# Kernel optimization log

Measured on AMD Instinct MI355X. Metric: run time of the kernel, lower is better.

The kernel has to match this reference:

```python
import jax, jax.numpy as jnp
import numpy as np

N, M, D = 16384, 1024, 1024


def setup_inputs() -> dict:
    key = jax.random.key(0)
    kq, kp = jax.random.split(key)
    query = jax.random.normal(kq, (N, D), dtype=jnp.float32)
    proto = jax.random.normal(kp, (M, D), dtype=jnp.float32)
    return {"query": query, "proto": proto}


def reference(query, proto):
    # Pairwise squared euclidean: ||q||^2 - 2 q.p + ||p||^2  (same math as
    # the expand+pow+sum in compute_euclidean, but without the [N,M,D] blowup).
    q2 = jnp.sum(query * query, axis=-1, keepdims=True)          # [N,1]
    p2 = jnp.sum(proto * proto, axis=-1)                          # [M]
    qp = jnp.einsum('nd,md->nm', query, proto)                    # [N,M]
    dists = q2 - 2.0 * qp + p2[None, :]                           # [N,M]
    # Original applies F.softmax(-dists, dim=1) (named log_p_y but is softmax).
    return jax.nn.softmax(-dists, axis=1)
```

## Files before the change

kernel.cpp:

```cpp
#include <hip/hip_runtime.h>
#include <stdint.h>

#define N_Q 16384
#define M_P 1024
#define D_K 1024

typedef __attribute__((ext_vector_type(8))) __bf16 bf16x8;
typedef __attribute__((ext_vector_type(4))) float floatx4;
typedef __attribute__((ext_vector_type(4))) unsigned int uint4v;

#define AS1 __attribute__((address_space(1)))
#define AS3 __attribute__((address_space(3)))

__device__ __forceinline__ unsigned short f2bf(float f) {
    unsigned int u = __float_as_uint(f);
    u += 0x7fffu + ((u >> 16) & 1u);
    return (unsigned short)(u >> 16);
}
__device__ __forceinline__ float bf2f(unsigned short h) {
    return __uint_as_float(((unsigned int)h) << 16);
}

__device__ __forceinline__ void split_chunk(floatx4 f0, floatx4 f1,
                                            uint4v* hi, uint4v* lo) {
    float e[8] = {f0.x, f0.y, f0.z, f0.w, f1.x, f1.y, f1.z, f1.w};
    unsigned int hb[4], lb[4];
#pragma unroll
    for (int p = 0; p < 4; ++p) {
        unsigned int u0 = __float_as_uint(e[2 * p]);
        unsigned int u1 = __float_as_uint(e[2 * p + 1]);
        hb[p] = __builtin_amdgcn_perm(u1, u0, 0x07060302);
        float l0 = e[2 * p]     - __uint_as_float(u0 & 0xffff0000u);
        float l1 = e[2 * p + 1] - __uint_as_float(u1 & 0xffff0000u);
        lb[p] = __builtin_amdgcn_perm(__float_as_uint(l1), __float_as_uint(l0),
                                      0x07060302);
    }
    uint4v h = {hb[0], hb[1], hb[2], hb[3]};
    uint4v l = {lb[0], lb[1], lb[2], lb[3]};
    *hi = h;
    *lo = l;
}

__global__ __launch_bounds__(256) void convert_proto_kernel(
    const float* __restrict__ proto, unsigned short* __restrict__ ph,
    unsigned short* __restrict__ pl, float* __restrict__ p2) {
    __shared__ float sred[4];
    int m = blockIdx.x;
    int t = threadIdx.x;
    size_t base4 = (size_t)m * (D_K / 4) + t;
    float4 v = ((const float4*)proto)[base4];
    ushort4 h, l;
    h.x = f2bf(v.x); l.x = f2bf(v.x - bf2f(h.x));
    h.y = f2bf(v.y); l.y = f2bf(v.y - bf2f(h.y));
    h.z = f2bf(v.z); l.z = f2bf(v.z - bf2f(h.z));
    h.w = f2bf(v.w); l.w = f2bf(v.w - bf2f(h.w));
    ((ushort4*)ph)[base4] = h;
    ((ushort4*)pl)[base4] = l;
    float sq = v.x * v.x + v.y * v.y + v.z * v.z + v.w * v.w;
#pragma unroll
    for (int off = 1; off < 64; off <<= 1) sq += __shfl_xor(sq, off);
    if ((t & 63) == 0) sred[t >> 6] = sq;
    __syncthreads();
    if (t == 0) p2[m] = sred[0] + sred[1] + sred[2] + sred[3];
}

__global__ __launch_bounds__(512, 2) void gemm_logits_kernel(
    const float* __restrict__ query,
    const unsigned short* __restrict__ ph, const unsigned short* __restrict__ pl,
    const float* __restrict__ p2, float* __restrict__ out) {
    __shared__ unsigned short sAh[2][16 * 512];
    __shared__ unsigned short sAl[2][16 * 512];
    __shared__ unsigned short sBh[2][16 * 512];
    __shared__ unsigned short sBl[2][16 * 512];

    const int tid = threadIdx.x;
    const int wave = tid >> 6;
    const int lane = tid & 63;
    const int wr = wave >> 2;
    const int wc = wave & 3;

    const int b = blockIdx.x;
    const int v = (b & 7) * 32 + (b >> 3);
    const int colt = v >> 6;
    const int rowt = v & 63;
    const int row0 = rowt * 256;
    const int col0 = colt * 256;

    const int rlB = lane >> 2;
    const int cioB = (lane & 3) ^ ((lane >> 3) & 3);
    const int halfB = wave >> 2;
    const int sgB = wave & 3;
    const unsigned short* gB = (halfB ? pl : ph)
        + (size_t)(col0 + sgB * 64 + rlB) * D_K + cioB * 8;

    const int rlA = lane >> 2;
    const int cA = lane & 3;
    const AS1 float* gA = (const AS1 float*)query
        + (size_t)(row0 + wave * 32 + rlA) * D_K + cA * 8;
    const int wroff = (4 * rlA + (cA ^ ((rlA >> 1) & 3))) * 8;

    const int rsel = lane & 15;
    const int kq = lane >> 4;
    const int fragoff = (4 * rsel + (kq ^ ((rsel >> 1) & 3))) * 8;

    floatx4 zero = {0.0f, 0.0f, 0.0f, 0.0f};
    floatx4 acc[8][4];
#pragma unroll
    for (int i = 0; i < 8; ++i)
#pragma unroll
        for (int j = 0; j < 4; ++j) acc[i][j] = zero;

    floatx4 f0[2], f1[2];
    bf16x8 bh[4], bl[4];
    bf16x8 ah[2][2], al[2][2];

    auto issueA = [&](int kb) {
#pragma unroll
        for (int s = 0; s < 2; ++s) {
            const AS1 float* p = gA + (size_t)(s * 16) * D_K + kb;
            f0[s] = *(const AS1 floatx4*)p;
            f1[s] = *(const AS1 floatx4*)(p + 4);
        }
    };
    auto issueB = [&](int kb, int nxt) {
        unsigned short* dstB = (halfB ? sBl[nxt] : sBh[nxt]) + sgB * 4 * 512;
#pragma unroll
        for (int s = 0; s < 4; ++s)
            __builtin_amdgcn_global_load_lds(
                (const AS1 unsigned int*)(const void*)(gB + (size_t)(s * 16) * D_K + kb),
                (AS3 unsigned int*)(void*)(dstB + s * 512), 16, 0, 0);
    };
    auto writeA = [&](int nxt, int s) {
        uint4v hi, lo;
        split_chunk(f0[s], f1[s], &hi, &lo);
        const int off = (wave * 2 + s) * 512 + wroff;
        *(uint4v*)(sAh[nxt] + off) = hi;
        *(uint4v*)(sAl[nxt] + off) = lo;
    };
    auto ldBfrag = [&](int cur) {
#pragma unroll
        for (int j = 0; j < 4; ++j) {
            const int boff = (wc * 4 + j) * 512 + fragoff;
            bh[j] = *(const bf16x8*)(sBh[cur] + boff);
            bl[j] = *(const bf16x8*)(sBl[cur] + boff);
        }
    };
    auto ldA = [&](int cur, int i0, int set) {
#pragma unroll
        for (int t = 0; t < 2; ++t) {
            const int aoff = (wr * 8 + i0 + t) * 512 + fragoff;
            ah[set][t] = *(const bf16x8*)(sAh[cur] + aoff);
            al[set][t] = *(const bf16x8*)(sAl[cur] + aoff);
        }
    };
    auto mfma2 = [&](int i0, int set) {
#pragma unroll
        for (int j = 0; j < 4; ++j)
#pragma unroll
            for (int t = 0; t < 2; ++t) {
                acc[i0 + t][j] = __builtin_amdgcn_mfma_f32_16x16x32_bf16(ah[set][t], bh[j], acc[i0 + t][j], 0, 0, 0);
                acc[i0 + t][j] = __builtin_amdgcn_mfma_f32_16x16x32_bf16(ah[set][t], bl[j], acc[i0 + t][j], 0, 0, 0);
                acc[i0 + t][j] = __builtin_amdgcn_mfma_f32_16x16x32_bf16(al[set][t], bh[j], acc[i0 + t][j], 0, 0, 0);
            }
    };

#define LGKM_MFMA(n, i0, set)                                   \
    asm volatile("s_waitcnt lgkmcnt(" #n ")" ::: "memory");     \
    __builtin_amdgcn_sched_barrier(0);                          \
    __builtin_amdgcn_s_setprio(1);                              \
    mfma2(i0, set);                                             \
    __builtin_amdgcn_s_setprio(0);

    auto stepf = [&](int kbnB, int kbnA, int cur, int nxt, bool pfB, bool pfA) {
        if (pfB) issueB(kbnB, nxt);
        ldBfrag(cur);
        ldA(cur, 0, 0);
        ldA(cur, 2, 1);
        LGKM_MFMA(4, 0, 0)
        ldA(cur, 4, 0);
        LGKM_MFMA(4, 2, 1)
        ldA(cur, 6, 1);
        LGKM_MFMA(4, 4, 0)
        if (pfB) { writeA(nxt, 0); writeA(nxt, 1); }
        if (pfA) issueA(kbnA);
        asm volatile("s_waitcnt lgkmcnt(0)" ::: "memory");
        if (pfB) {
            if (pfA) asm volatile("s_waitcnt vmcnt(4)" ::: "memory");
            else     asm volatile("s_waitcnt vmcnt(0)" ::: "memory");
        }
        __builtin_amdgcn_sched_barrier(0);
        __builtin_amdgcn_s_setprio(1);
        mfma2(6, 1);
        __builtin_amdgcn_s_setprio(0);
        __builtin_amdgcn_s_barrier();
    };

    issueA(0);
    issueB(0, 0);
    writeA(0, 0);
    writeA(0, 1);
    issueA(32);
    asm volatile("s_waitcnt lgkmcnt(0)" ::: "memory");
    asm volatile("s_waitcnt vmcnt(4)" ::: "memory");
    __builtin_amdgcn_s_barrier();

    for (int kt = 0; kt < 30; kt += 2) {
        stepf((kt + 1) * 32, (kt + 2) * 32, 0, 1, true, true);
        stepf((kt + 2) * 32, (kt + 3) * 32, 1, 0, true, true);
    }
    stepf(31 * 32, 0, 0, 1, true, false);
    stepf(0, 0, 1, 0, false, false);

#undef LGKM_MFMA

#pragma unroll
    for (int j = 0; j < 4; ++j) {
        const int gc = col0 + wc * 64 + j * 16 + rsel;
        const float p2v = p2[gc];
#pragma unroll
        for (int i = 0; i < 8; ++i) {
            const int gr = row0 + wr * 128 + i * 16 + kq * 4;
#pragma unroll
            for (int r = 0; r < 4; ++r) {
                out[(size_t)(gr + r) * M_P + gc] = 2.0f * acc[i][j][r] - p2v;
            }
        }
    }
}

__global__ __launch_bounds__(256) void naive_logits_kernel(
    const float* __restrict__ query, const float* __restrict__ proto,
    float* __restrict__ out) {
    __shared__ float qs[D_K];
    int n = blockIdx.x;
    int t = threadIdx.x;
    ((float4*)qs)[t] = ((const float4*)(query + (size_t)n * D_K))[t];
    __syncthreads();
    float acc[4] = {0.f, 0.f, 0.f, 0.f};
    float pp[4] = {0.f, 0.f, 0.f, 0.f};
    for (int d = 0; d < D_K; d += 4) {
        float4 qv = *(const float4*)(qs + d);
#pragma unroll
        for (int j = 0; j < 4; ++j) {
            const float4 pv = *(const float4*)(proto + (size_t)(t + 256 * j) * D_K + d);
            acc[j] += qv.x * pv.x + qv.y * pv.y + qv.z * pv.z + qv.w * pv.w;
            pp[j] += pv.x * pv.x + pv.y * pv.y + pv.z * pv.z + pv.w * pv.w;
        }
    }
#pragma unroll
    for (int j = 0; j < 4; ++j)
        out[(size_t)n * M_P + t + 256 * j] = 2.0f * acc[j] - pp[j];
}

__global__ __launch_bounds__(256) void softmax_kernel(float* __restrict__ out) {
    const int lane = threadIdx.x & 63;
    int n = blockIdx.x * 4 + (threadIdx.x >> 6);
    for (int it = 0; it < 2; ++it, n += 8192) {
        float* row = out + (size_t)n * M_P;
        floatx4 v[4];
#pragma unroll
        for (int k = 0; k < 4; ++k)
            v[k] = *((const floatx4*)row + k * 64 + lane);
        float mx = fmaxf(fmaxf(v[0].x, v[0].y), fmaxf(v[0].z, v[0].w));
#pragma unroll
        for (int k = 1; k < 4; ++k)
            mx = fmaxf(mx, fmaxf(fmaxf(v[k].x, v[k].y), fmaxf(v[k].z, v[k].w)));
#pragma unroll
        for (int off = 1; off < 64; off <<= 1) mx = fmaxf(mx, __shfl_xor(mx, off));
        float s = 0.0f;
#pragma unroll
        for (int k = 0; k < 4; ++k) {
            v[k].x = __expf(v[k].x - mx);
            v[k].y = __expf(v[k].y - mx);
            v[k].z = __expf(v[k].z - mx);
            v[k].w = __expf(v[k].w - mx);
            s += v[k].x + v[k].y + v[k].z + v[k].w;
        }
#pragma unroll
        for (int off = 1; off < 64; off <<= 1) s += __shfl_xor(s, off);
        const float inv = 1.0f / s;
#pragma unroll
        for (int k = 0; k < 4; ++k) {
            floatx4 o;
            o.x = v[k].x * inv; o.y = v[k].y * inv;
            o.z = v[k].z * inv; o.w = v[k].w * inv;
            __builtin_nontemporal_store(o, (floatx4*)row + k * 64 + lane);
        }
    }
}

extern "C" void kernel_launch(void* const* d_in, const int* in_sizes, int n_in,
                              void* d_out, int out_size, void* d_ws, size_t ws_size,
                              hipStream_t stream) {
    const float* query = (const float*)d_in[0];
    const float* proto = (const float*)d_in[1];
    float* out = (float*)d_out;

    const size_t pElems = (size_t)M_P * D_K;
    const size_t needed = pElems * 2 * 2 + M_P * 4;

    if (ws_size >= needed) {
        unsigned short* ph = (unsigned short*)d_ws;
        unsigned short* pl = ph + pElems;
        float* p2 = (float*)(pl + pElems);

        convert_proto_kernel<<<M_P, 256, 0, stream>>>(proto, ph, pl, p2);
        gemm_logits_kernel<<<(N_Q / 256) * (M_P / 256), 512, 0, stream>>>(
            query, ph, pl, p2, out);
    } else {
        naive_logits_kernel<<<N_Q, 256, 0, stream>>>(query, proto, out);
    }
    softmax_kernel<<<2048, 256, 0, stream>>>(out);
}
```

Before: 198.1 us.

## Triple-buffer B tiles in LDS to prefetch two k-steps ahead

```diff
diff --git a/kernel.cpp b/kernel.cpp
--- a/kernel.cpp
+++ b/kernel.cpp
@@ -70,8 +70,8 @@
     const float* __restrict__ p2, float* __restrict__ out) {
     __shared__ unsigned short sAh[2][16 * 512];
     __shared__ unsigned short sAl[2][16 * 512];
-    __shared__ unsigned short sBh[2][16 * 512];
-    __shared__ unsigned short sBl[2][16 * 512];
+    __shared__ unsigned short sBh[3][16 * 512];
+    __shared__ unsigned short sBl[3][16 * 512];
 
     const int tid = threadIdx.x;
     const int wave = tid >> 6;
@@ -122,8 +122,8 @@
             f1[s] = *(const AS1 floatx4*)(p + 4);
         }
     };
-    auto issueB = [&](int kb, int nxt) {
-        unsigned short* dstB = (halfB ? sBl[nxt] : sBh[nxt]) + sgB * 4 * 512;
+    auto issueB = [&](int kb, int dst) {
+        unsigned short* dstB = (halfB ? sBl[dst] : sBh[dst]) + sgB * 4 * 512;
 #pragma unroll
         for (int s = 0; s < 4; ++s)
             __builtin_amdgcn_global_load_lds(
@@ -137,12 +137,12 @@
         *(uint4v*)(sAh[nxt] + off) = hi;
         *(uint4v*)(sAl[nxt] + off) = lo;
     };
-    auto ldBfrag = [&](int cur) {
+    auto ldBfrag = [&](int curB) {
 #pragma unroll
         for (int j = 0; j < 4; ++j) {
             const int boff = (wc * 4 + j) * 512 + fragoff;
-            bh[j] = *(const bf16x8*)(sBh[cur] + boff);
-            bl[j] = *(const bf16x8*)(sBl[cur] + boff);
+            bh[j] = *(const bf16x8*)(sBh[curB] + boff);
+            bl[j] = *(const bf16x8*)(sBl[curB] + boff);
         }
     };
     auto ldA = [&](int cur, int i0, int set) {
@@ -171,45 +171,52 @@
     mfma2(i0, set);                                             \
     __builtin_amdgcn_s_setprio(0);
 
-    auto stepf = [&](int kbnB, int kbnA, int cur, int nxt, bool pfB, bool pfA) {
-        if (pfB) issueB(kbnB, nxt);
-        ldBfrag(cur);
-        ldA(cur, 0, 0);
-        ldA(cur, 2, 1);
+    auto stepf = [&](int kb2, int curA, int nxtA, int curB, int dstB,
+                     bool pfB2, bool pfA2, bool pfW) {
+        if (pfB2) issueB(kb2, dstB);
+        ldBfrag(curB);
+        ldA(curA, 0, 0);
+        ldA(curA, 2, 1);
         LGKM_MFMA(4, 0, 0)
-        ldA(cur, 4, 0);
+        ldA(curA, 4, 0);
         LGKM_MFMA(4, 2, 1)
-        ldA(cur, 6, 1);
+        ldA(curA, 6, 1);
         LGKM_MFMA(4, 4, 0)
-        if (pfB) { writeA(nxt, 0); writeA(nxt, 1); }
-        if (pfA) issueA(kbnA);
-        asm volatile("s_waitcnt lgkmcnt(0)" ::: "memory");
-        if (pfB) {
-            if (pfA) asm volatile("s_waitcnt vmcnt(4)" ::: "memory");
-            else     asm volatile("s_waitcnt vmcnt(0)" ::: "memory");
-        }
+        if (pfW) { writeA(nxtA, 0); writeA(nxtA, 1); }
+        if (pfA2) issueA(kb2);
+        if (pfW) { asm volatile("s_waitcnt lgkmcnt(4)" ::: "memory"); }
+        else     { asm volatile("s_waitcnt lgkmcnt(0)" ::: "memory"); }
         __builtin_amdgcn_sched_barrier(0);
         __builtin_amdgcn_s_setprio(1);
         mfma2(6, 1);
         __builtin_amdgcn_s_setprio(0);
+        asm volatile("s_waitcnt lgkmcnt(0)" ::: "memory");
+        if (pfB2)      { asm volatile("s_waitcnt vmcnt(8)" ::: "memory"); }
+        else if (pfW)  { asm volatile("s_waitcnt vmcnt(0)" ::: "memory"); }
         __builtin_amdgcn_s_barrier();
     };
 
+    issueB(0, 0);
+    issueB(32, 1);
     issueA(0);
-    issueB(0, 0);
     writeA(0, 0);
     writeA(0, 1);
     issueA(32);
     asm volatile("s_waitcnt lgkmcnt(0)" ::: "memory");
-    asm volatile("s_waitcnt vmcnt(4)" ::: "memory");
+    asm volatile("s_waitcnt vmcnt(8)" ::: "memory");
     __builtin_amdgcn_s_barrier();
 
-    for (int kt = 0; kt < 30; kt += 2) {
-        stepf((kt + 1) * 32, (kt + 2) * 32, 0, 1, true, true);
-        stepf((kt + 2) * 32, (kt + 3) * 32, 1, 0, true, true);
-    }
-    stepf(31 * 32, 0, 0, 1, true, false);
-    stepf(0, 0, 1, 0, false, false);
+    for (int kt = 0; kt < 30; kt += 6) {
+        const int kb = kt * 32;
+        stepf(kb + 2 * 32, 0, 1, 0, 2, true, true, true);
+        stepf(kb + 3 * 32, 1, 0, 1, 0, true, true, true);
+        stepf(kb + 4 * 32, 0, 1, 2, 1, true, true, true);
+        stepf(kb + 5 * 32, 1, 0, 0, 2, true, true, true);
+        stepf(kb + 6 * 32, 0, 1, 1, 0, true, true, true);
+        stepf(kb + 7 * 32, 1, 0, 2, 1, true, true, true);
+    }
+    stepf(0, 0, 1, 0, 2, false, false, true);
+    stepf(0, 1, 0, 1, 0, false, false, false);
 
 #undef LGKM_MFMA
 
```

New measurement: 196.7 us. Within noise of the previous version (-0.7%).

## Switch GEMM inner loop from 16x16x32 to 32x32x16 bf16 MFMA tiles

Applied to the files above, without the earlier changes.

```diff
diff --git a/kernel.cpp b/kernel.cpp
--- a/kernel.cpp
+++ b/kernel.cpp
@@ -7,6 +7,7 @@
 
 typedef __attribute__((ext_vector_type(8))) __bf16 bf16x8;
 typedef __attribute__((ext_vector_type(4))) float floatx4;
+typedef __attribute__((ext_vector_type(16))) float floatx16;
 typedef __attribute__((ext_vector_type(4))) unsigned int uint4v;
 
 #define AS1 __attribute__((address_space(1)))
@@ -99,19 +100,21 @@
         + (size_t)(row0 + wave * 32 + rlA) * D_K + cA * 8;
     const int wroff = (4 * rlA + (cA ^ ((rlA >> 1) & 3))) * 8;
 
-    const int rsel = lane & 15;
-    const int kq = lane >> 4;
-    const int fragoff = (4 * rsel + (kq ^ ((rsel >> 1) & 3))) * 8;
-
-    floatx4 zero = {0.0f, 0.0f, 0.0f, 0.0f};
-    floatx4 acc[8][4];
-#pragma unroll
-    for (int i = 0; i < 8; ++i)
-#pragma unroll
-        for (int j = 0; j < 4; ++j) acc[i][j] = zero;
+    const int r32 = lane & 31;
+    const int rl16 = lane & 15;
+    const int subsel = (lane & 31) >> 4;
+    const int ghalf = lane >> 5;
+
+    floatx16 acc[4][2];
+#pragma unroll
+    for (int i = 0; i < 4; ++i)
+#pragma unroll
+        for (int j = 0; j < 2; ++j)
+#pragma unroll
+            for (int r = 0; r < 16; ++r) acc[i][j][r] = 0.0f;
 
     floatx4 f0[2], f1[2];
-    bf16x8 bh[4], bl[4];
+    bf16x8 bh[2][2], bl[2][2];
     bf16x8 ah[2][2], al[2][2];
 
     auto issueA = [&](int kb) {
@@ -137,61 +140,71 @@
         *(uint4v*)(sAh[nxt] + off) = hi;
         *(uint4v*)(sAl[nxt] + off) = lo;
     };
+    auto fragoff32 = [&](int s0, int kh) {
+        const int g = kh * 2 + ghalf;
+        return (s0 + subsel) * 512 + (4 * rl16 + (g ^ ((rl16 >> 1) & 3))) * 8;
+    };
     auto ldBfrag = [&](int cur) {
 #pragma unroll
-        for (int j = 0; j < 4; ++j) {
-            const int boff = (wc * 4 + j) * 512 + fragoff;
-            bh[j] = *(const bf16x8*)(sBh[cur] + boff);
-            bl[j] = *(const bf16x8*)(sBl[cur] + boff);
-        }
-    };
-    auto ldA = [&](int cur, int i0, int set) {
-#pragma unroll
-        for (int t = 0; t < 2; ++t) {
-            const int aoff = (wr * 8 + i0 + t) * 512 + fragoff;
-            ah[set][t] = *(const bf16x8*)(sAh[cur] + aoff);
-            al[set][t] = *(const bf16x8*)(sAl[cur] + aoff);
-        }
-    };
-    auto mfma2 = [&](int i0, int set) {
-#pragma unroll
-        for (int j = 0; j < 4; ++j)
-#pragma unroll
-            for (int t = 0; t < 2; ++t) {
-                acc[i0 + t][j] = __builtin_amdgcn_mfma_f32_16x16x32_bf16(ah[set][t], bh[j], acc[i0 + t][j], 0, 0, 0);
-                acc[i0 + t][j] = __builtin_amdgcn_mfma_f32_16x16x32_bf16(ah[set][t], bl[j], acc[i0 + t][j], 0, 0, 0);
-                acc[i0 + t][j] = __builtin_amdgcn_mfma_f32_16x16x32_bf16(al[set][t], bh[j], acc[i0 + t][j], 0, 0, 0);
+        for (int tj = 0; tj < 2; ++tj)
+#pragma unroll
+            for (int kh = 0; kh < 2; ++kh) {
+                const int off = fragoff32(wc * 4 + tj * 2, kh);
+                bh[tj][kh] = *(const bf16x8*)(sBh[cur] + off);
+                bl[tj][kh] = *(const bf16x8*)(sBl[cur] + off);
             }
     };
-
-#define LGKM_MFMA(n, i0, set)                                   \
+    auto ldA = [&](int cur, int tp, int kh, int set) {
+#pragma unroll
+        for (int u = 0; u < 2; ++u) {
+            const int ti = tp * 2 + u;
+            const int off = fragoff32(wr * 8 + ti * 2, kh);
+            ah[set][u] = *(const bf16x8*)(sAh[cur] + off);
+            al[set][u] = *(const bf16x8*)(sAl[cur] + off);
+        }
+    };
+    auto mfmaC = [&](int tp, int kh, int set) {
+#pragma unroll
+        for (int tj = 0; tj < 2; ++tj)
+#pragma unroll
+            for (int u = 0; u < 2; ++u) {
+                const int ti = tp * 2 + u;
+                acc[ti][tj] = __builtin_amdgcn_mfma_f32_32x32x16_bf16(ah[set][u], bh[tj][kh], acc[ti][tj], 0, 0, 0);
+                acc[ti][tj] = __builtin_amdgcn_mfma_f32_32x32x16_bf16(ah[set][u], bl[tj][kh], acc[ti][tj], 0, 0, 0);
+                acc[ti][tj] = __builtin_amdgcn_mfma_f32_32x32x16_bf16(al[set][u], bh[tj][kh], acc[ti][tj], 0, 0, 0);
+            }
+    };
+
+#define LGKM_MFMA(n, tp, kh, set)                               \
     asm volatile("s_waitcnt lgkmcnt(" #n ")" ::: "memory");     \
     __builtin_amdgcn_sched_barrier(0);                          \
     __builtin_amdgcn_s_setprio(1);                              \
-    mfma2(i0, set);                                             \
+    mfmaC(tp, kh, set);                                         \
     __builtin_amdgcn_s_setprio(0);
 
-    auto stepf = [&](int kbnB, int kbnA, int cur, int nxt, bool pfB, bool pfA) {
-        if (pfB) issueB(kbnB, nxt);
+    auto stepf = [&](int kbB, int kbA, int cur, int nxt, bool pfB, bool pfA) {
+        if (pfB) issueB(kbB, nxt);
         ldBfrag(cur);
-        ldA(cur, 0, 0);
-        ldA(cur, 2, 1);
-        LGKM_MFMA(4, 0, 0)
-        ldA(cur, 4, 0);
-        LGKM_MFMA(4, 2, 1)
-        ldA(cur, 6, 1);
-        LGKM_MFMA(4, 4, 0)
+        ldA(cur, 0, 0, 0);
+        ldA(cur, 1, 0, 1);
+        LGKM_MFMA(4, 0, 0, 0)
+        ldA(cur, 0, 1, 0);
+        LGKM_MFMA(4, 1, 0, 1)
+        ldA(cur, 1, 1, 1);
+        LGKM_MFMA(4, 0, 1, 0)
         if (pfB) { writeA(nxt, 0); writeA(nxt, 1); }
-        if (pfA) issueA(kbnA);
+        if (pfA) issueA(kbA);
+        if (pfB) { asm volatile("s_waitcnt lgkmcnt(4)" ::: "memory"); }
+        else     { asm volatile("s_waitcnt lgkmcnt(0)" ::: "memory"); }
+        __builtin_amdgcn_sched_barrier(0);
+        __builtin_amdgcn_s_setprio(1);
+        mfmaC(1, 1, 1);
+        __builtin_amdgcn_s_setprio(0);
         asm volatile("s_waitcnt lgkmcnt(0)" ::: "memory");
         if (pfB) {
-            if (pfA) asm volatile("s_waitcnt vmcnt(4)" ::: "memory");
-            else     asm volatile("s_waitcnt vmcnt(0)" ::: "memory");
-        }
-        __builtin_amdgcn_sched_barrier(0);
-        __builtin_amdgcn_s_setprio(1);
-        mfma2(6, 1);
-        __builtin_amdgcn_s_setprio(0);
+            if (pfA) { asm volatile("s_waitcnt vmcnt(4)" ::: "memory"); }
+            else     { asm volatile("s_waitcnt vmcnt(0)" ::: "memory"); }
+        }
         __builtin_amdgcn_s_barrier();
     };
 
@@ -214,15 +227,16 @@
 #undef LGKM_MFMA
 
 #pragma unroll
-    for (int j = 0; j < 4; ++j) {
-        const int gc = col0 + wc * 64 + j * 16 + rsel;
+    for (int tj = 0; tj < 2; ++tj) {
+        const int gc = col0 + wc * 64 + tj * 32 + r32;
         const float p2v = p2[gc];
 #pragma unroll
-        for (int i = 0; i < 8; ++i) {
-            const int gr = row0 + wr * 128 + i * 16 + kq * 4;
-#pragma unroll
-            for (int r = 0; r < 4; ++r) {
-                out[(size_t)(gr + r) * M_P + gc] = 2.0f * acc[i][j][r] - p2v;
+        for (int ti = 0; ti < 4; ++ti) {
+            const int rbase = row0 + wr * 128 + ti * 32 + 4 * ghalf;
+#pragma unroll
+            for (int reg = 0; reg < 16; ++reg) {
+                const int gr = rbase + (reg & 3) + 8 * (reg >> 2);
+                out[(size_t)gr * M_P + gc] = 2.0f * acc[ti][tj][reg] - p2v;
             }
         }
     }
```

Measured after the change: 210.3 us. +6.1%, slower.

## Fuse proto conversion, GEMM and softmax into one cooperative kernel

Applied to the files above, without the earlier changes.

```diff
diff --git a/kernel.cpp b/kernel.cpp
--- a/kernel.cpp
+++ b/kernel.cpp
@@ -1,5 +1,8 @@
 #include <hip/hip_runtime.h>
+#include <hip/hip_cooperative_groups.h>
 #include <stdint.h>
+
+namespace cg = cooperative_groups;
 
 #define N_Q 16384
 #define M_P 1024
@@ -39,6 +42,259 @@
     uint4v l = {lb[0], lb[1], lb[2], lb[3]};
     *hi = h;
     *lo = l;
+}
+
+__device__ __forceinline__ void gemm_body(
+    const float* __restrict__ query,
+    const unsigned short* __restrict__ ph, const unsigned short* __restrict__ pl,
+    const float* __restrict__ p2, float* __restrict__ out,
+    unsigned short (*sAh)[16 * 512], unsigned short (*sAl)[16 * 512],
+    unsigned short (*sBh)[16 * 512], unsigned short (*sBl)[16 * 512]) {
+    const int tid = threadIdx.x;
+    const int wave = tid >> 6;
+    const int lane = tid & 63;
+    const int wr = wave >> 2;
+    const int wc = wave & 3;
+
+    const int b = blockIdx.x;
+    const int v = (b & 7) * 32 + (b >> 3);
+    const int colt = v >> 6;
+    const int rowt = v & 63;
+    const int row0 = rowt * 256;
+    const int col0 = colt * 256;
+
+    const int rlB = lane >> 2;
+    const int cioB = (lane & 3) ^ ((lane >> 3) & 3);
+    const int halfB = wave >> 2;
+    const int sgB = wave & 3;
+    const unsigned short* gB = (halfB ? pl : ph)
+        + (size_t)(col0 + sgB * 64 + rlB) * D_K + cioB * 8;
+
+    const int rlA = lane >> 2;
+    const int cA = lane & 3;
+    const AS1 float* gA = (const AS1 float*)query
+        + (size_t)(row0 + wave * 32 + rlA) * D_K + cA * 8;
+    const int wroff = (4 * rlA + (cA ^ ((rlA >> 1) & 3))) * 8;
+
+    const int rsel = lane & 15;
+    const int kq = lane >> 4;
+    const int fragoff = (4 * rsel + (kq ^ ((rsel >> 1) & 3))) * 8;
+
+    floatx4 zero = {0.0f, 0.0f, 0.0f, 0.0f};
+    floatx4 acc[8][4];
+#pragma unroll
+    for (int i = 0; i < 8; ++i)
+#pragma unroll
+        for (int j = 0; j < 4; ++j) acc[i][j] = zero;
+
+    floatx4 f0[2], f1[2];
+    bf16x8 bh[4], bl[4];
+    bf16x8 ah[2][2], al[2][2];
+
+    auto issueA = [&](int kb) {
+#pragma unroll
+        for (int s = 0; s < 2; ++s) {
+            const AS1 float* p = gA + (size_t)(s * 16) * D_K + kb;
+            f0[s] = *(const AS1 floatx4*)p;
+            f1[s] = *(const AS1 floatx4*)(p + 4);
+        }
+    };
+    auto issueB = [&](int kb, int nxt) {
+        unsigned short* dstB = (halfB ? sBl[nxt] : sBh[nxt]) + sgB * 4 * 512;
+#pragma unroll
+        for (int s = 0; s < 4; ++s)
+            __builtin_amdgcn_global_load_lds(
+                (const AS1 unsigned int*)(const void*)(gB + (size_t)(s * 16) * D_K + kb),
+                (AS3 unsigned int*)(void*)(dstB + s * 512), 16, 0, 0);
+    };
+    auto writeA = [&](int nxt, int s) {
+        uint4v hi, lo;
+        split_chunk(f0[s], f1[s], &hi, &lo);
+        const int off = (wave * 2 + s) * 512 + wroff;
+        *(uint4v*)(sAh[nxt] + off) = hi;
+        *(uint4v*)(sAl[nxt] + off) = lo;
+    };
+    auto ldBfrag = [&](int cur) {
+#pragma unroll
+        for (int j = 0; j < 4; ++j) {
+            const int boff = (wc * 4 + j) * 512 + fragoff;
+            bh[j] = *(const bf16x8*)(sBh[cur] + boff);
+            bl[j] = *(const bf16x8*)(sBl[cur] + boff);
+        }
+    };
+    auto ldA = [&](int cur, int i0, int set) {
+#pragma unroll
+        for (int t = 0; t < 2; ++t) {
+            const int aoff = (wr * 8 + i0 + t) * 512 + fragoff;
+            ah[set][t] = *(const bf16x8*)(sAh[cur] + aoff);
+            al[set][t] = *(const bf16x8*)(sAl[cur] + aoff);
+        }
+    };
+    auto mfma2 = [&](int i0, int set) {
+#pragma unroll
+        for (int j = 0; j < 4; ++j)
+#pragma unroll
+            for (int t = 0; t < 2; ++t) {
+                acc[i0 + t][j] = __builtin_amdgcn_mfma_f32_16x16x32_bf16(ah[set][t], bh[j], acc[i0 + t][j], 0, 0, 0);
+                acc[i0 + t][j] = __builtin_amdgcn_mfma_f32_16x16x32_bf16(ah[set][t], bl[j], acc[i0 + t][j], 0, 0, 0);
+                acc[i0 + t][j] = __builtin_amdgcn_mfma_f32_16x16x32_bf16(al[set][t], bh[j], acc[i0 + t][j], 0, 0, 0);
+            }
+    };
+
+#define LGKM_MFMA(n, i0, set)                                   \
+    asm volatile("s_waitcnt lgkmcnt(" #n ")" ::: "memory");     \
+    __builtin_amdgcn_sched_barrier(0);                          \
+    __builtin_amdgcn_s_setprio(1);                              \
+    mfma2(i0, set);                                             \
+    __builtin_amdgcn_s_setprio(0);
+
+    auto stepf = [&](int kbB, int kbA, int cur, int nxt, bool pfB, bool pfA) {
+        if (pfB) issueB(kbB, nxt);
+        ldBfrag(cur);
+        ldA(cur, 0, 0);
+        ldA(cur, 2, 1);
+        LGKM_MFMA(4, 0, 0)
+        ldA(cur, 4, 0);
+        LGKM_MFMA(4, 2, 1)
+        ldA(cur, 6, 1);
+        LGKM_MFMA(4, 4, 0)
+        if (pfB) { writeA(nxt, 0); writeA(nxt, 1); }
+        if (pfA) issueA(kbA);
+        if (pfB) { asm volatile("s_waitcnt lgkmcnt(4)" ::: "memory"); }
+        else     { asm volatile("s_waitcnt lgkmcnt(0)" ::: "memory"); }
+        __builtin_amdgcn_sched_barrier(0);
+        __builtin_amdgcn_s_setprio(1);
+        mfma2(6, 1);
+        __builtin_amdgcn_s_setprio(0);
+        asm volatile("s_waitcnt lgkmcnt(0)" ::: "memory");
+        if (pfB) {
+            if (pfA) { asm volatile("s_waitcnt vmcnt(4)" ::: "memory"); }
+            else     { asm volatile("s_waitcnt vmcnt(0)" ::: "memory"); }
+        }
+        __builtin_amdgcn_s_barrier();
+    };
+
+    issueA(0);
+    issueB(0, 0);
+    writeA(0, 0);
+    writeA(0, 1);
+    issueA(32);
+    asm volatile("s_waitcnt lgkmcnt(0)" ::: "memory");
+    asm volatile("s_waitcnt vmcnt(4)" ::: "memory");
+    __builtin_amdgcn_s_barrier();
+
+    for (int kt = 0; kt < 30; kt += 2) {
+        stepf((kt + 1) * 32, (kt + 2) * 32, 0, 1, true, true);
+        stepf((kt + 2) * 32, (kt + 3) * 32, 1, 0, true, true);
+    }
+    stepf(31 * 32, 0, 0, 1, true, false);
+    stepf(0, 0, 1, 0, false, false);
+
+#undef LGKM_MFMA
+
+#pragma unroll
+    for (int j = 0; j < 4; ++j) {
+        const int gc = col0 + wc * 64 + j * 16 + rsel;
+        const float p2v = p2[gc];
+#pragma unroll
+        for (int i = 0; i < 8; ++i) {
+            const int gr = row0 + wr * 128 + i * 16 + kq * 4;
+#pragma unroll
+            for (int r = 0; r < 4; ++r) {
+                out[(size_t)(gr + r) * M_P + gc] = 2.0f * acc[i][j][r] - p2v;
+            }
+        }
+    }
+}
+
+__device__ __forceinline__ void softmax_row(float* __restrict__ row, int lane) {
+    floatx4 v[4];
+#pragma unroll
+    for (int k = 0; k < 4; ++k)
+        v[k] = *((const floatx4*)row + k * 64 + lane);
+    float mx = fmaxf(fmaxf(v[0].x, v[0].y), fmaxf(v[0].z, v[0].w));
+#pragma unroll
+    for (int k = 1; k < 4; ++k)
+        mx = fmaxf(mx, fmaxf(fmaxf(v[k].x, v[k].y), fmaxf(v[k].z, v[k].w)));
+#pragma unroll
+    for (int off = 1; off < 64; off <<= 1) mx = fmaxf(mx, __shfl_xor(mx, off));
+    float s = 0.0f;
+#pragma unroll
+    for (int k = 0; k < 4; ++k) {
+        v[k].x = __expf(v[k].x - mx);
+        v[k].y = __expf(v[k].y - mx);
+        v[k].z = __expf(v[k].z - mx);
+        v[k].w = __expf(v[k].w - mx);
+        s += v[k].x + v[k].y + v[k].z + v[k].w;
+    }
+#pragma unroll
+    for (int off = 1; off < 64; off <<= 1) s += __shfl_xor(s, off);
+    const float inv = 1.0f / s;
+#pragma unroll
+    for (int k = 0; k < 4; ++k) {
+        floatx4 o;
+        o.x = v[k].x * inv; o.y = v[k].y * inv;
+        o.z = v[k].z * inv; o.w = v[k].w * inv;
+        __builtin_nontemporal_store(o, (floatx4*)row + k * 64 + lane);
+    }
+}
+
+__global__ __launch_bounds__(512, 2) void fused_kernel(
+    const float* __restrict__ query, const float* __restrict__ proto,
+    unsigned short* __restrict__ ph, unsigned short* __restrict__ pl,
+    float* __restrict__ p2, float* __restrict__ out) {
+    __shared__ unsigned short sAh[2][16 * 512];
+    __shared__ unsigned short sAl[2][16 * 512];
+    __shared__ unsigned short sBh[2][16 * 512];
+    __shared__ unsigned short sBl[2][16 * 512];
+    __shared__ float sred[8];
+
+    const int tid = threadIdx.x;
+
+    {
+        const int r = blockIdx.x * 4 + (tid >> 7);
+        const int c = tid & 127;
+        const size_t base4 = (size_t)r * (D_K / 4) + c * 2;
+        const float4 v0 = ((const float4*)proto)[base4];
+        const float4 v1 = ((const float4*)proto)[base4 + 1];
+        ushort4 h0, l0, h1, l1;
+        h0.x = f2bf(v0.x); l0.x = f2bf(v0.x - bf2f(h0.x));
+        h0.y = f2bf(v0.y); l0.y = f2bf(v0.y - bf2f(h0.y));
+        h0.z = f2bf(v0.z); l0.z = f2bf(v0.z - bf2f(h0.z));
+        h0.w = f2bf(v0.w); l0.w = f2bf(v0.w - bf2f(h0.w));
+        h1.x = f2bf(v1.x); l1.x = f2bf(v1.x - bf2f(h1.x));
+        h1.y = f2bf(v1.y); l1.y = f2bf(v1.y - bf2f(h1.y));
+        h1.z = f2bf(v1.z); l1.z = f2bf(v1.z - bf2f(h1.z));
+        h1.w = f2bf(v1.w); l1.w = f2bf(v1.w - bf2f(h1.w));
+        ((ushort4*)ph)[base4] = h0; ((ushort4*)ph)[base4 + 1] = h1;
+        ((ushort4*)pl)[base4] = l0; ((ushort4*)pl)[base4 + 1] = l1;
+        float sq = v0.x * v0.x + v0.y * v0.y + v0.z * v0.z + v0.w * v0.w
+                 + v1.x * v1.x + v1.y * v1.y + v1.z * v1.z + v1.w * v1.w;
+#pragma unroll
+        for (int off = 1; off < 64; off <<= 1) sq += __shfl_xor(sq, off);
+        if ((tid & 63) == 0) sred[tid >> 6] = sq;
+        __syncthreads();
+        if (tid < 4) p2[blockIdx.x * 4 + tid] = sred[2 * tid] + sred[2 * tid + 1];
+    }
+    __threadfence();
+    cg::this_grid().sync();
+    __threadfence();
+
+    gemm_body(query, ph, pl, p2, out, sAh, sAl, sBh, sBl);
+
+    __threadfence();
+    cg::this_grid().sync();
+    __threadfence();
+
+    {
+        const int lane = tid & 63;
+        const int w = tid >> 6;
+#pragma unroll
+        for (int it = 0; it < 8; ++it) {
+            const int n = blockIdx.x * 64 + it * 8 + w;
+            softmax_row(out + (size_t)n * M_P, lane);
+        }
+    }
 }
 
 __global__ __launch_bounds__(256) void convert_proto_kernel(
@@ -72,159 +328,14 @@
     __shared__ unsigned short sAl[2][16 * 512];
     __shared__ unsigned short sBh[2][16 * 512];
     __shared__ unsigned short sBl[2][16 * 512];
-
-    const int tid = threadIdx.x;
-    const int wave = tid >> 6;
-    const int lane = tid & 63;
-    const int wr = wave >> 2;
-    const int wc = wave & 3;
-
-    const int b = blockIdx.x;
-    const int v = (b & 7) * 32 + (b >> 3);
-    const int colt = v >> 6;
-    const int rowt = v & 63;
-    const int row0 = rowt * 256;
-    const int col0 = colt * 256;
-
-    const int rlB = lane >> 2;
-    const int cioB = (lane & 3) ^ ((lane >> 3) & 3);
-    const int halfB = wave >> 2;
-    const int sgB = wave & 3;
-    const unsigned short* gB = (halfB ? pl : ph)
-        + (size_t)(col0 + sgB * 64 + rlB) * D_K + cioB * 8;
-
-    const int rlA = lane >> 2;
-    const int cA = lane & 3;
-    const AS1 float* gA = (const AS1 float*)query
-        + (size_t)(row0 + wave * 32 + rlA) * D_K + cA * 8;
-    const int wroff = (4 * rlA + (cA ^ ((rlA >> 1) & 3))) * 8;
-
-    const int rsel = lane & 15;
-    const int kq = lane >> 4;
-    const int fragoff = (4 * rsel + (kq ^ ((rsel >> 1) & 3))) * 8;
-
-    floatx4 zero = {0.0f, 0.0f, 0.0f, 0.0f};
-    floatx4 acc[8][4];
-#pragma unroll
-    for (int i = 0; i < 8; ++i)
-#pragma unroll
-        for (int j = 0; j < 4; ++j) acc[i][j] = zero;
-
-    floatx4 f0[2], f1[2];
-    bf16x8 bh[4], bl[4];
-    bf16x8 ah[2][2], al[2][2];
-
-    auto issueA = [&](int kb) {
-#pragma unroll
-        for (int s = 0; s < 2; ++s) {
-            const AS1 float* p = gA + (size_t)(s * 16) * D_K + kb;
-            f0[s] = *(const AS1 floatx4*)p;
-            f1[s] = *(const AS1 floatx4*)(p + 4);
-        }
-    };
-    auto issueB = [&](int kb, int nxt) {
-        unsigned short* dstB = (halfB ? sBl[nxt] : sBh[nxt]) + sgB * 4 * 512;
-#pragma unroll
-        for (int s = 0; s < 4; ++s)
-            __builtin_amdgcn_global_load_lds(
-                (const AS1 unsigned int*)(const void*)(gB + (size_t)(s * 16) * D_K + kb),
-                (AS3 unsigned int*)(void*)(dstB + s * 512), 16, 0, 0);
-    };
-    auto writeA = [&](int nxt, int s) {
-        uint4v hi, lo;
-        split_chunk(f0[s], f1[s], &hi, &lo);
-        const int off = (wave * 2 + s) * 512 + wroff;
-        *(uint4v*)(sAh[nxt] + off) = hi;
-        *(uint4v*)(sAl[nxt] + off) = lo;
-    };
-    auto ldBfrag = [&](int cur) {
-#pragma unroll
-        for (int j = 0; j < 4; ++j) {
-            const int boff = (wc * 4 + j) * 512 + fragoff;
-            bh[j] = *(const bf16x8*)(sBh[cur] + boff);
-            bl[j] = *(const bf16x8*)(sBl[cur] + boff);
-        }
-    };
-    auto ldA = [&](int cur, int i0, int set) {
-#pragma unroll
-        for (int t = 0; t < 2; ++t) {
-            const int aoff = (wr * 8 + i0 + t) * 512 + fragoff;
-            ah[set][t] = *(const bf16x8*)(sAh[cur] + aoff);
-            al[set][t] = *(const bf16x8*)(sAl[cur] + aoff);
-        }
-    };
-    auto mfma2 = [&](int i0, int set) {
-#pragma unroll
-        for (int j = 0; j < 4; ++j)
-#pragma unroll
-            for (int t = 0; t < 2; ++t) {
-                acc[i0 + t][j] = __builtin_amdgcn_mfma_f32_16x16x32_bf16(ah[set][t], bh[j], acc[i0 + t][j], 0, 0, 0);
-                acc[i0 + t][j] = __builtin_amdgcn_mfma_f32_16x16x32_bf16(ah[set][t], bl[j], acc[i0 + t][j], 0, 0, 0);
-                acc[i0 + t][j] = __builtin_amdgcn_mfma_f32_16x16x32_bf16(al[set][t], bh[j], acc[i0 + t][j], 0, 0, 0);
-            }
-    };
-
-#define LGKM_MFMA(n, i0, set)                                   \
-    asm volatile("s_waitcnt lgkmcnt(" #n ")" ::: "memory");     \
-    __builtin_amdgcn_sched_barrier(0);                          \
-    __builtin_amdgcn_s_setprio(1);                              \
-    mfma2(i0, set);                                             \
-    __builtin_amdgcn_s_setprio(0);
-
-    auto stepf = [&](int kbnB, int kbnA, int cur, int nxt, bool pfB, bool pfA) {
-        if (pfB) issueB(kbnB, nxt);
-        ldBfrag(cur);
-        ldA(cur, 0, 0);
-        ldA(cur, 2, 1);
-        LGKM_MFMA(4, 0, 0)
-        ldA(cur, 4, 0);
-        LGKM_MFMA(4, 2, 1)
-        ldA(cur, 6, 1);
-        LGKM_MFMA(4, 4, 0)
-        if (pfB) { writeA(nxt, 0); writeA(nxt, 1); }
-        if (pfA) issueA(kbnA);
-        asm volatile("s_waitcnt lgkmcnt(0)" ::: "memory");
-        if (pfB) {
-            if (pfA) asm volatile("s_waitcnt vmcnt(4)" ::: "memory");
-            else     asm volatile("s_waitcnt vmcnt(0)" ::: "memory");
-        }
-        __builtin_amdgcn_sched_barrier(0);
-        __builtin_amdgcn_s_setprio(1);
-        mfma2(6, 1);
-        __builtin_amdgcn_s_setprio(0);
-        __builtin_amdgcn_s_barrier();
-    };
-
-    issueA(0);
-    issueB(0, 0);
-    writeA(0, 0);
-    writeA(0, 1);
-    issueA(32);
-    asm volatile("s_waitcnt lgkmcnt(0)" ::: "memory");
-    asm volatile("s_waitcnt vmcnt(4)" ::: "memory");
-    __builtin_amdgcn_s_barrier();
-
-    for (int kt = 0; kt < 30; kt += 2) {
-        stepf((kt + 1) * 32, (kt + 2) * 32, 0, 1, true, true);
-        stepf((kt + 2) * 32, (kt + 3) * 32, 1, 0, true, true);
-    }
-    stepf(31 * 32, 0, 0, 1, true, false);
-    stepf(0, 0, 1, 0, false, false);
-
-#undef LGKM_MFMA
-
-#pragma unroll
-    for (int j = 0; j < 4; ++j) {
-        const int gc = col0 + wc * 64 + j * 16 + rsel;
-        const float p2v = p2[gc];
-#pragma unroll
-        for (int i = 0; i < 8; ++i) {
-            const int gr = row0 + wr * 128 + i * 16 + kq * 4;
-#pragma unroll
-            for (int r = 0; r < 4; ++r) {
-                out[(size_t)(gr + r) * M_P + gc] = 2.0f * acc[i][j][r] - p2v;
-            }
-        }
+    gemm_body(query, ph, pl, p2, out, sAh, sAl, sBh, sBl);
+}
+
+__global__ __launch_bounds__(256) void softmax_kernel(float* __restrict__ out) {
+    const int lane = threadIdx.x & 63;
+    int n = blockIdx.x * 4 + (threadIdx.x >> 6);
+    for (int it = 0; it < 2; ++it, n += 8192) {
+        softmax_row(out + (size_t)n * M_P, lane);
     }
 }
 
@@ -252,43 +363,6 @@
         out[(size_t)n * M_P + t + 256 * j] = 2.0f * acc[j] - pp[j];
 }
 
-__global__ __launch_bounds__(256) void softmax_kernel(float* __restrict__ out) {
-    const int lane = threadIdx.x & 63;
-    int n = blockIdx.x * 4 + (threadIdx.x >> 6);
-    for (int it = 0; it < 2; ++it, n += 8192) {
-        float* row = out + (size_t)n * M_P;
-        floatx4 v[4];
-#pragma unroll
-        for (int k = 0; k < 4; ++k)
-            v[k] = *((const floatx4*)row + k * 64 + lane);
-        float mx = fmaxf(fmaxf(v[0].x, v[0].y), fmaxf(v[0].z, v[0].w));
-#pragma unroll
-        for (int k = 1; k < 4; ++k)
-            mx = fmaxf(mx, fmaxf(fmaxf(v[k].x, v[k].y), fmaxf(v[k].z, v[k].w)));
-#pragma unroll
-        for (int off = 1; off < 64; off <<= 1) mx = fmaxf(mx, __shfl_xor(mx, off));
-        float s = 0.0f;
-#pragma unroll
-        for (int k = 0; k < 4; ++k) {
-            v[k].x = __expf(v[k].x - mx);
-            v[k].y = __expf(v[k].y - mx);
-            v[k].z = __expf(v[k].z - mx);
-            v[k].w = __expf(v[k].w - mx);
-            s += v[k].x + v[k].y + v[k].z + v[k].w;
-        }
-#pragma unroll
-        for (int off = 1; off < 64; off <<= 1) s += __shfl_xor(s, off);
-        const float inv = 1.0f / s;
-#pragma unroll
-        for (int k = 0; k < 4; ++k) {
-            floatx4 o;
-            o.x = v[k].x * inv; o.y = v[k].y * inv;
-            o.z = v[k].z * inv; o.w = v[k].w * inv;
-            __builtin_nontemporal_store(o, (floatx4*)row + k * 64 + lane);
-        }
-    }
-}
-
 extern "C" void kernel_launch(void* const* d_in, const int* in_sizes, int n_in,
                               void* d_out, int out_size, void* d_ws, size_t ws_size,
                               hipStream_t stream) {
@@ -304,11 +378,18 @@
         unsigned short* pl = ph + pElems;
         float* p2 = (float*)(pl + pElems);
 
-        convert_proto_kernel<<<M_P, 256, 0, stream>>>(proto, ph, pl, p2);
-        gemm_logits_kernel<<<(N_Q / 256) * (M_P / 256), 512, 0, stream>>>(
-            query, ph, pl, p2, out);
+        void* args[] = {(void*)&query, (void*)&proto, (void*)&ph,
+                        (void*)&pl,    (void*)&p2,    (void*)&out};
+        hipError_t e = hipLaunchCooperativeKernel(
+            (const void*)fused_kernel, dim3(256), dim3(512), args, 0, stream);
+        if (e != hipSuccess) {
+            convert_proto_kernel<<<M_P, 256, 0, stream>>>(proto, ph, pl, p2);
+            gemm_logits_kernel<<<(N_Q / 256) * (M_P / 256), 512, 0, stream>>>(
+                query, ph, pl, p2, out);
+            softmax_kernel<<<N_Q / 8, 256, 0, stream>>>(out);
+        }
     } else {
         naive_logits_kernel<<<N_Q, 256, 0, stream>>>(query, proto, out);
-    }
-    softmax_kernel<<<2048, 256, 0, stream>>>(out);
-}
+        softmax_kernel<<<N_Q / 8, 256, 0, stream>>>(out);
+    }
+}
```

New measurement: 426.6 us. 115% more time.
